# Optimization experiments

Measured on AMD Instinct MI355X. Metric: run time of the kernel, lower is better.

Reference implementation:

```python
import jax, jax.numpy as jnp
import numpy as np

N = 100000   # nodes
E = 1600000  # edges (avg degree 16)
Q = 64       # mesoscale velocity bins
H = 64       # collision MLP hidden dim
DT = 0.1
REG = 1e-6


def setup_inputs() -> dict:
    key = jax.random.key(0)
    ks = jax.random.split(key, 10)
    return {
        "f": jax.random.uniform(ks[0], (N, Q), jnp.float32),
        "macro_u": jax.random.normal(ks[1], (N, 1), jnp.float32),
        "source": 0.01 * jax.random.normal(ks[2], (N, Q), jnp.float32),
        "edge_src": jax.random.randint(ks[3], (E,), 0, N, jnp.int32),
        "edge_dst": jax.random.randint(ks[4], (E,), 0, N, jnp.int32),
        "edge_w": jax.random.uniform(ks[5], (E,), jnp.float32),
        "xi": jnp.linspace(-1.0, 1.0, Q).astype(jnp.float32),
        "w_in": jax.random.normal(ks[6], (Q, H), jnp.float32) / np.float32(np.sqrt(Q)),
        "b_in": jnp.zeros((H,), jnp.float32),
        "w_hid": jax.random.normal(ks[7], (3, H, H), jnp.float32) / np.float32(np.sqrt(H)),
        "b_hid": jnp.zeros((3, H), jnp.float32),
        "w_out": jax.random.normal(ks[8], (H, Q), jnp.float32) / np.float32(np.sqrt(H)),
        "b_out": jnp.zeros((Q,), jnp.float32),
    }


def _collision(f, macro_u, xi, w_in, b_in, w_hid, b_hid, w_out, b_out):
    # 5-layer MLP: relu hidden, tanh output (CollisionOperator.forward)
    x = jax.nn.relu(f @ w_in + b_in)
    for i in range(3):  # fixed small layer count, not a data-dim loop
        x = jax.nn.relu(x @ w_hid[i] + b_hid[i])
    omega = jnp.tanh(x @ w_out + b_out)                     # [N, Q]
    # Hard collision-invariance constraint: Omega* = (I - C^T (C C^T)^-1 C) Omega
    q = f.shape[1]
    w = jnp.full((q,), 1.0 / q, f.dtype)                    # quadrature weights
    xi_shifted = xi[None, :] + macro_u                      # [N, Q]
    C = jnp.stack([jnp.broadcast_to(w, xi_shifted.shape), w * xi_shifted], axis=1)  # [N,2,Q]
    CCT = jnp.einsum('naq,nbq->nab', C, C) + REG * jnp.eye(2, dtype=f.dtype)        # [N,2,2]
    v = jnp.einsum('naq,nq->na', C, omega)                  # [N,2]
    s = jnp.linalg.solve(CCT, v[..., None])[..., 0]         # [N,2]  (== CCT^-1 v)
    return omega - jnp.einsum('naq,na->nq', C, s)           # avoid dense [N,Q,Q] projection


def _transport(f, xi, edge_src, edge_dst, edge_w, n):
    # BoltzmannUpdater.compute_transport_term: both inflow (on graph) and
    # outflow (on reverse graph) reduce to the same per-edge message
    #   m_e = (w_e / out_deg[src_e]) * xi * (f[dst_e] - f[src_e])
    # aggregated at dst (inflow) and at src (outflow); transport = outflow - inflow.
    out_deg = jax.ops.segment_sum(jnp.ones_like(edge_w), edge_src, num_segments=n)
    q_e = edge_w / out_deg[edge_src]                         # [E]
    msg = q_e[:, None] * xi[None, :] * (f[edge_dst] - f[edge_src])  # [E, Q]
    inflow = jax.ops.segment_sum(msg, edge_dst, num_segments=n)
    outflow = jax.ops.segment_sum(msg, edge_src, num_segments=n)
    return outflow - inflow


def reference(f, macro_u, source, edge_src, edge_dst, edge_w, xi,
              w_in, b_in, w_hid, b_hid, w_out, b_out):
    f = jnp.maximum(f, 0.0)  # clamp(min=0)
    omega = _collision(f, macro_u, xi, w_in, b_in, w_hid, b_hid, w_out, b_out)
    trans = _transport(f, xi, edge_src, edge_dst, edge_w, f.shape[0])
    f_new = f - DT * (trans - omega - source)
    return jnp.maximum(f_new, 0.0)
```

## Files before the change

kernel.cpp:

```cpp
#include <hip/hip_runtime.h>

#define NN 100000
#define EE 1600000
#define DTc 0.1f
#define REGc 1e-6f
#define WQc (1.0f / 64.0f)

#define NB 782
#define CAP 4736
#define BCHUNK 16384
#define BS_NB 98
#define ACT_S 72
#define PRE_NB 3125
#define WP_NB 80
#define SIDE_BIT (1u << 24)

typedef unsigned long long u64;
typedef __attribute__((ext_vector_type(8))) short short8;
typedef __attribute__((ext_vector_type(4))) float f32x4;

__device__ __forceinline__ unsigned short f2bf(float x) {
    unsigned u = __float_as_uint(x);
    unsigned r = (u + 0x7fffu + ((u >> 16) & 1u)) >> 16;
    return (unsigned short)r;
}
__device__ __forceinline__ float bf2f(unsigned short s) {
    return __uint_as_float(((unsigned)s) << 16);
}
__device__ __forceinline__ unsigned pack2(float a, float b) {
    return (unsigned)f2bf(fmaxf(a, 0.f)) | ((unsigned)f2bf(fmaxf(b, 0.f)) << 16);
}

__global__ __launch_bounds__(256) void prep_kernel(
    const float* __restrict__ f, unsigned int* __restrict__ fb16u,
    const float* __restrict__ w_in, const float* __restrict__ w_hid,
    const float* __restrict__ w_out, unsigned short* __restrict__ wp,
    const int* __restrict__ esrc, const int* __restrict__ edst,
    const float* __restrict__ ew, int* __restrict__ bcur,
    u64* __restrict__ adj64) {
    int b = blockIdx.x;
    if (b < BS_NB) {
        __shared__ int cnt[NB];
        __shared__ int bas[NB];
        int t = threadIdx.x;
        for (int j = t; j < NB; j += 256) cnt[j] = 0;
        __syncthreads();
        int base = b * BCHUNK;
        int nE = min(BCHUNK, EE - base);
#pragma unroll
        for (int k = 0; k < 8; k++) {
            int i = k * 2048 + t * 8;
            if (i < nE) {
                int4 sa = *(const int4*)&esrc[base + i];
                int4 sb = *(const int4*)&esrc[base + i + 4];
                int4 da = *(const int4*)&edst[base + i];
                int4 db = *(const int4*)&edst[base + i + 4];
                atomicAdd(&cnt[sa.x >> 7], 1); atomicAdd(&cnt[da.x >> 7], 1);
                atomicAdd(&cnt[sa.y >> 7], 1); atomicAdd(&cnt[da.y >> 7], 1);
                atomicAdd(&cnt[sa.z >> 7], 1); atomicAdd(&cnt[da.z >> 7], 1);
                atomicAdd(&cnt[sa.w >> 7], 1); atomicAdd(&cnt[da.w >> 7], 1);
                atomicAdd(&cnt[sb.x >> 7], 1); atomicAdd(&cnt[db.x >> 7], 1);
                atomicAdd(&cnt[sb.y >> 7], 1); atomicAdd(&cnt[db.y >> 7], 1);
                atomicAdd(&cnt[sb.z >> 7], 1); atomicAdd(&cnt[db.z >> 7], 1);
                atomicAdd(&cnt[sb.w >> 7], 1); atomicAdd(&cnt[db.w >> 7], 1);
            }
        }
        __syncthreads();
        for (int j = t; j < NB; j += 256) {
            int c = cnt[j];
            bas[j] = (c ? atomicAdd(&bcur[j], c) : 0) + j * CAP;
            cnt[j] = 0;
        }
        __syncthreads();
#pragma unroll
        for (int k = 0; k < 8; k++) {
            int i = k * 2048 + t * 8;
            if (i < nE) {
                int4 sa = *(const int4*)&esrc[base + i];
                int4 sb = *(const int4*)&esrc[base + i + 4];
                int4 da = *(const int4*)&edst[base + i];
                int4 db = *(const int4*)&edst[base + i + 4];
                float4 wa = *(const float4*)&ew[base + i];
                float4 wb = *(const float4*)&ew[base + i + 4];
#define EMIT(s, d, w)                                                         \
                {                                                             \
                    u64 wb64 = ((u64)__float_as_uint(w)) << 32;               \
                    int p1 = bas[(s) >> 7] + atomicAdd(&cnt[(s) >> 7], 1);    \
                    adj64[p1] = wb64 | SIDE_BIT | (unsigned)((d) | (((s) & 127) << 17)); \
                    int p2 = bas[(d) >> 7] + atomicAdd(&cnt[(d) >> 7], 1);    \
                    adj64[p2] = wb64 | (unsigned)((s) | (((d) & 127) << 17)); \
                }
                EMIT(sa.x, da.x, wa.x) EMIT(sa.y, da.y, wa.y)
                EMIT(sa.z, da.z, wa.z) EMIT(sa.w, da.w, wa.w)
                EMIT(sb.x, db.x, wb.x) EMIT(sb.y, db.y, wb.y)
                EMIT(sb.z, db.z, wb.z) EMIT(sb.w, db.w, wb.w)
#undef EMIT
            }
        }
    } else if (b < BS_NB + PRE_NB) {
        int i = (b - BS_NB) * 256 + threadIdx.x;
        float4 v0 = *(const float4*)&f[i * 8];
        float4 v1 = *(const float4*)&f[i * 8 + 4];
        uint4 w;
        w.x = pack2(v0.x, v0.y);
        w.y = pack2(v0.z, v0.w);
        w.z = pack2(v1.x, v1.y);
        w.w = pack2(v1.z, v1.w);
        *(uint4*)&fb16u[i * 4] = w;
    } else {
        int i = (b - BS_NB - PRE_NB) * 256 + threadIdx.x;
        int l = i >> 12, idx = i & 4095;
        int n = idx >> 6, k = idx & 63;
        const float* W = (l == 0) ? w_in : (l < 4 ? w_hid + (l - 1) * 4096 : w_out);
        wp[i] = f2bf(W[k * 64 + n]);
    }
}

__global__ __launch_bounds__(256) void bucket_histo(
    const int* __restrict__ bcur, const u64* __restrict__ adj64,
    int* __restrict__ node_offs, int* __restrict__ node_end,
    int* __restrict__ deg) {
    __shared__ int cnt_tot[128], cnt_src[128], sc[128];
    int t = threadIdx.x, b = blockIdx.x;
    if (t < 128) { cnt_tot[t] = 0; cnt_src[t] = 0; }
    __syncthreads();
    int used = bcur[b];
    int gstart = b * CAP;
    for (int i = t; i < used; i += 256) {
        unsigned lo = (unsigned)adj64[gstart + i];
        int local = (lo >> 17) & 127;
        atomicAdd(&cnt_tot[local], 1);
        if (lo & SIDE_BIT) atomicAdd(&cnt_src[local], 1);
    }
    __syncthreads();
    if (t < 128) sc[t] = cnt_tot[t];
    __syncthreads();
    for (int o = 1; o < 128; o <<= 1) {
        int x = 0;
        if (t < 128 && t >= o) x = sc[t - o];
        __syncthreads();
        if (t < 128) sc[t] += x;
        __syncthreads();
    }
    if (t < 128) {
        int n = b * 128 + t;
        if (n < NN) {
            node_offs[n] = gstart + sc[t] - cnt_tot[t];
            node_end[n]  = gstart + sc[t];
            deg[n] = cnt_src[t];
        }
    }
}

__global__ __launch_bounds__(256) void bucket_scatter(
    const int* __restrict__ bcur, const u64* __restrict__ adj64,
    const int* __restrict__ node_offs, const int* __restrict__ deg,
    unsigned int* __restrict__ adj4) {
    __shared__ int cur[128];
    __shared__ float ldeg[128];
    int t = threadIdx.x, b = blockIdx.x;
    if (t < 128) {
        int n = b * 128 + t;
        cur[t] = (n < NN) ? node_offs[n] : 0;
        ldeg[t] = (n < NN) ? (float)deg[n] : 1.f;
    }
    __syncthreads();
    int used = bcur[b];
    int gstart = b * CAP;
    for (int i = t; i < used; i += 256) {
        u64 e = adj64[gstart + i];
        unsigned lo = (unsigned)e;
        int local = (lo >> 17) & 127;
        unsigned other = lo & 0x1FFFFu;
        float w = __uint_as_float((unsigned)(e >> 32));
        float dv = (lo & SIDE_BIT) ? ldeg[local] : (float)deg[other];
        float q = w / dv;
        unsigned q15 = (unsigned)(q * 32768.f + 0.5f);
        if (q15 > 32767u) q15 = 32767u;
        int p = atomicAdd(&cur[local], 1);
        adj4[p] = (q15 << 17) | other;
    }
}

#define ACC8(q, r)                                          \
    a0 = fmaf(q, __uint_as_float(r.x << 16), a0);           \
    a1 = fmaf(q, __uint_as_float(r.x & 0xFFFF0000u), a1);   \
    a2 = fmaf(q, __uint_as_float(r.y << 16), a2);           \
    a3 = fmaf(q, __uint_as_float(r.y & 0xFFFF0000u), a3);   \
    a4 = fmaf(q, __uint_as_float(r.z << 16), a4);           \
    a5 = fmaf(q, __uint_as_float(r.z & 0xFFFF0000u), a5);   \
    a6 = fmaf(q, __uint_as_float(r.w << 16), a6);           \
    a7 = fmaf(q, __uint_as_float(r.w & 0xFFFF0000u), a7);   \
    qs += q;

__global__ __launch_bounds__(256) void gather_kernel(
    const unsigned int* __restrict__ fb16u, const int* __restrict__ node_offs,
    const int* __restrict__ node_end,
    const unsigned int* __restrict__ adj, const float* __restrict__ xi,
    float* __restrict__ trans) {
    const float QS = 1.f / 32768.f;
    int lane = threadIdx.x & 63;
    int n = blockIdx.x * 4 + (threadIdx.x >> 6);
    if (n >= NN) return;
    int c = lane & 7;
    int qt = lane >> 3;
    int j = node_offs[n];
    int end = node_end[n];
    float a0 = 0.f, a1 = 0.f, a2 = 0.f, a3 = 0.f;
    float a4 = 0.f, a5 = 0.f, a6 = 0.f, a7 = 0.f, qs = 0.f;
    for (; j + 32 <= end; j += 32) {
        unsigned e0 = __builtin_nontemporal_load(&adj[j + qt]);
        unsigned e1 = __builtin_nontemporal_load(&adj[j + 8 + qt]);
        unsigned e2 = __builtin_nontemporal_load(&adj[j + 16 + qt]);
        unsigned e3 = __builtin_nontemporal_load(&adj[j + 24 + qt]);
        uint4 r0 = *(const uint4*)&fb16u[(e0 & 0x1FFFFu) * 32 + c * 4];
        uint4 r1 = *(const uint4*)&fb16u[(e1 & 0x1FFFFu) * 32 + c * 4];
        uint4 r2 = *(const uint4*)&fb16u[(e2 & 0x1FFFFu) * 32 + c * 4];
        uint4 r3 = *(const uint4*)&fb16u[(e3 & 0x1FFFFu) * 32 + c * 4];
        float q0 = (float)(e0 >> 17) * QS;
        float q1 = (float)(e1 >> 17) * QS;
        float q2 = (float)(e2 >> 17) * QS;
        float q3 = (float)(e3 >> 17) * QS;
        ACC8(q0, r0)
        ACC8(q1, r1)
        ACC8(q2, r2)
        ACC8(q3, r3)
    }
    for (; j + 8 <= end; j += 8) {
        unsigned e = __builtin_nontemporal_load(&adj[j + qt]);
        uint4 r = *(const uint4*)&fb16u[(e & 0x1FFFFu) * 32 + c * 4];
        float q = (float)(e >> 17) * QS;
        ACC8(q, r)
    }
    if (j < end) {
        int idx = j + qt;
        bool ok = idx < end;
        unsigned e = ok ? adj[idx] : 0u;
        uint4 r = *(const uint4*)&fb16u[(e & 0x1FFFFu) * 32 + c * 4];
        float q = ok ? (float)(e >> 17) * QS : 0.f;
        ACC8(q, r)
    }
#define RED3(x) x += __shfl_xor(x, 8); x += __shfl_xor(x, 16); x += __shfl_xor(x, 32)
    RED3(a0); RED3(a1); RED3(a2); RED3(a3);
    RED3(a4); RED3(a5); RED3(a6); RED3(a7); RED3(qs);
    if (qt == 0) {
        uint4 rn = *(const uint4*)&fb16u[n * 32 + c * 4];
        float4 x0 = *(const float4*)&xi[c * 8];
        float4 x1 = *(const float4*)&xi[c * 8 + 4];
        f32x4 o0, o1;
        o0.x = x0.x * (a0 - qs * __uint_as_float(rn.x << 16));
        o0.y = x0.y * (a1 - qs * __uint_as_float(rn.x & 0xFFFF0000u));
        o0.z = x0.z * (a2 - qs * __uint_as_float(rn.y << 16));
        o0.w = x0.w * (a3 - qs * __uint_as_float(rn.y & 0xFFFF0000u));
        o1.x = x1.x * (a4 - qs * __uint_as_float(rn.z << 16));
        o1.y = x1.y * (a5 - qs * __uint_as_float(rn.z & 0xFFFF0000u));
        o1.z = x1.z * (a6 - qs * __uint_as_float(rn.w << 16));
        o1.w = x1.w * (a7 - qs * __uint_as_float(rn.w & 0xFFFF0000u));
        __builtin_nontemporal_store(o0, (f32x4*)&trans[n * 64 + c * 8]);
        __builtin_nontemporal_store(o1, (f32x4*)&trans[n * 64 + c * 8 + 4]);
    }
}

__global__ __launch_bounds__(256) void node_kernel(
    const unsigned short* __restrict__ fb16, const float* __restrict__ f,
    const float* __restrict__ macro_u, const float* __restrict__ source,
    const float* __restrict__ xi, const unsigned short* __restrict__ wp,
    const float* __restrict__ b_in, const float* __restrict__ b_hid,
    const float* __restrict__ b_out,
    const float* __restrict__ trans, float* __restrict__ out) {
    __shared__ __attribute__((aligned(16))) unsigned short act[128 * ACT_S];
    __shared__ float s0s[128], s1s[128], us[128], xif[64];

    const int t = threadIdx.x;
    const int wid = t >> 6;
    const int lane = t & 63;
    const int m = lane & 15;
    const int quad = lane >> 4;
    const int nodeBase = blockIdx.x * 128;
    const int gbase = nodeBase * 64;

    if (t < 128) {
        int n = nodeBase + t;
        us[t] = (n < NN) ? macro_u[n] : 0.f;
    }
    if (t < 64) xif[t] = xi[t];

#pragma unroll
    for (int i = 0; i < 8; i++) {
        int r = wid * 32 + i * 4 + (lane >> 4);
        int c = (lane & 15) * 4;
        uint2 v = {0u, 0u};
        if (nodeBase + r < NN) v = *(const uint2*)&fb16[gbase + r * 64 + c];
        *(uint2*)&act[r * ACT_S + c] = v;
    }

    const int rowbase = wid * 32;

    for (int l = 0; l < 5; l++) {
        const unsigned short* W = wp + l * 4096;
        const float* B = (l == 0) ? b_in : (l < 4 ? b_hid + (l - 1) * 64 : b_out);

        short8 Af[2][2], Bf[4][2];
#pragma unroll
        for (int rt = 0; rt < 2; rt++)
#pragma unroll
            for (int kk = 0; kk < 2; kk++)
                Af[rt][kk] = *(const short8*)&act[(rowbase + rt * 16 + m) * ACT_S + kk * 32 + quad * 8];
#pragma unroll
        for (int ct = 0; ct < 4; ct++)
#pragma unroll
            for (int kk = 0; kk < 2; kk++)
                Bf[ct][kk] = *(const short8*)&W[(ct * 16 + m) * 64 + kk * 32 + quad * 8];

        f32x4 acc[2][4];
#pragma unroll
        for (int rt = 0; rt < 2; rt++)
#pragma unroll
            for (int ct = 0; ct < 4; ct++) {
                acc[rt][ct] = (f32x4){0.f, 0.f, 0.f, 0.f};
                acc[rt][ct] = __builtin_amdgcn_mfma_f32_16x16x32_bf16(Af[rt][0], Bf[ct][0], acc[rt][ct], 0, 0, 0);
                acc[rt][ct] = __builtin_amdgcn_mfma_f32_16x16x32_bf16(Af[rt][1], Bf[ct][1], acc[rt][ct], 0, 0, 0);
            }

#pragma unroll
        for (int rt = 0; rt < 2; rt++)
#pragma unroll
            for (int ct = 0; ct < 4; ct++) {
                float bv = B[ct * 16 + m];
#pragma unroll
                for (int r = 0; r < 4; r++) {
                    int row = rowbase + rt * 16 + quad * 4 + r;
                    float val = acc[rt][ct][r] + bv;
                    val = (l < 4) ? fmaxf(val, 0.f) : tanhf(val);
                    act[row * ACT_S + ct * 16 + m] = f2bf(val);
                }
            }
    }
    __syncthreads();

    if (t < 128) {
        float u = us[t];
        float v0 = 0.f, v1 = 0.f, sxs2 = 0.f, sxi = 0.f;
        const short8* rp = (const short8*)&act[t * ACT_S];
#pragma unroll
        for (int c = 0; c < 8; c++) {
            short8 v = rp[c];
#pragma unroll
            for (int jj = 0; jj < 8; jj++) {
                float om = bf2f((unsigned short)v[jj]);
                float xv = xif[c * 8 + jj];
                float xs = xv + u;
                v0 += om;
                v1 += xs * om;
                sxs2 += xs * xs;
                sxi += xv;
            }
        }
        v0 *= WQc;
        v1 *= WQc;
        float c00 = WQc + REGc;
        float c01 = WQc * WQc * (sxi + 64.f * u);
        float c11 = WQc * WQc * sxs2 + REGc;
        float det = c00 * c11 - c01 * c01;
        float inv = 1.0f / det;
        s0s[t] = (c11 * v0 - c01 * v1) * inv;
        s1s[t] = (c00 * v1 - c01 * v0) * inv;
    }
    __syncthreads();

#pragma unroll
    for (int i = 0; i < 8; i++) {
        int e = (i * 256 + t) * 4;
        int nl = e >> 6;
        if (nodeBase + nl < NN) {
            int g = gbase + e;
            int c0 = e & 63;
            float4 fv = *(const float4*)&f[g];
            float4 sv = *(const float4*)&source[g];
            float4 tv = *(const float4*)&trans[g];
            float uu = us[nl];
            float sv0 = s0s[nl], sv1 = s1s[nl];
            float4 ov;
            float* ovp = (float*)&ov;
            const float* fp = (const float*)&fv;
            const float* sp = (const float*)&sv;
            const float* tp = (const float*)&tv;
#pragma unroll
            for (int jj = 0; jj < 4; jj++) {
                float om = bf2f(act[nl * ACT_S + c0 + jj]);
                float xs = xif[c0 + jj] + uu;
                float omst = om - WQc * (sv0 + xs * sv1);
                float val = fmaxf(fp[jj], 0.f) + DTc * (sp[jj] + omst - tp[jj]);
                ovp[jj] = fmaxf(val, 0.f);
            }
            *(float4*)&out[g] = ov;
        }
    }
}

extern "C" void kernel_launch(void* const* d_in, const int* in_sizes, int n_in,
                              void* d_out, int out_size, void* d_ws, size_t ws_size,
                              hipStream_t stream) {
    const float* f       = (const float*)d_in[0];
    const float* macro_u = (const float*)d_in[1];
    const float* source  = (const float*)d_in[2];
    const int*   esrc    = (const int*)d_in[3];
    const int*   edst    = (const int*)d_in[4];
    const float* ew      = (const float*)d_in[5];
    const float* xi      = (const float*)d_in[6];
    const float* w_in    = (const float*)d_in[7];
    const float* b_in    = (const float*)d_in[8];
    const float* w_hid   = (const float*)d_in[9];
    const float* b_hid   = (const float*)d_in[10];
    const float* w_out   = (const float*)d_in[11];
    const float* b_out   = (const float*)d_in[12];
    float* out = (float*)d_out;

    u64* adj64 = (u64*)d_ws;
    unsigned int* adj4 = (unsigned int*)(adj64 + (size_t)NB * CAP);
    int* deg   = (int*)(adj4 + (size_t)NB * CAP);
    int* node_offs = deg + NN;
    int* node_end  = node_offs + NN;
    int* bcur  = node_end + NN;
    float* trans = (float*)(bcur + 784);
    unsigned short* fb16 = (unsigned short*)(trans + (size_t)NN * 64);
    unsigned short* wp = fb16 + (size_t)NN * 64;

    hipMemsetAsync(bcur, 0, 784 * sizeof(int), stream);

    prep_kernel<<<BS_NB + PRE_NB + WP_NB, 256, 0, stream>>>(
        f, (unsigned int*)fb16, w_in, w_hid, w_out, wp, esrc, edst, ew, bcur, adj64);
    bucket_histo<<<NB, 256, 0, stream>>>(bcur, adj64, node_offs, node_end, deg);
    bucket_scatter<<<NB, 256, 0, stream>>>(bcur, adj64, node_offs, deg, adj4);
    gather_kernel<<<(NN + 3) / 4, 256, 0, stream>>>((const unsigned int*)fb16,
                                                    node_offs, node_end, adj4, xi, trans);
    node_kernel<<<(NN + 127) / 128, 256, 0, stream>>>(
        fb16, f, macro_u, source, xi, wp, b_in, b_hid, b_out, trans, out);
}
```

Measured before the change: 320.1 us.

## Store transport term in bf16 and split edge records into SoA arrays

```diff
diff --git a/kernel.cpp b/kernel.cpp
--- a/kernel.cpp
+++ b/kernel.cpp
@@ -18,6 +18,7 @@
 typedef unsigned long long u64;
 typedef __attribute__((ext_vector_type(8))) short short8;
 typedef __attribute__((ext_vector_type(4))) float f32x4;
+typedef __attribute__((ext_vector_type(4))) unsigned int u32x4;
 
 __device__ __forceinline__ unsigned short f2bf(float x) {
     unsigned u = __float_as_uint(x);
@@ -29,6 +30,9 @@
 }
 __device__ __forceinline__ unsigned pack2(float a, float b) {
     return (unsigned)f2bf(fmaxf(a, 0.f)) | ((unsigned)f2bf(fmaxf(b, 0.f)) << 16);
+}
+__device__ __forceinline__ unsigned pack2raw(float a, float b) {
+    return (unsigned)f2bf(a) | ((unsigned)f2bf(b) << 16);
 }
 
 __global__ __launch_bounds__(256) void prep_kernel(
@@ -37,7 +41,7 @@
     const float* __restrict__ w_out, unsigned short* __restrict__ wp,
     const int* __restrict__ esrc, const int* __restrict__ edst,
     const float* __restrict__ ew, int* __restrict__ bcur,
-    u64* __restrict__ adj64) {
+    unsigned int* __restrict__ lo4, float* __restrict__ w4) {
     int b = blockIdx.x;
     if (b < BS_NB) {
         __shared__ int cnt[NB];
@@ -84,11 +88,12 @@
                 float4 wb = *(const float4*)&ew[base + i + 4];
 #define EMIT(s, d, w)                                                         \
                 {                                                             \
-                    u64 wb64 = ((u64)__float_as_uint(w)) << 32;               \
                     int p1 = bas[(s) >> 7] + atomicAdd(&cnt[(s) >> 7], 1);    \
-                    adj64[p1] = wb64 | SIDE_BIT | (unsigned)((d) | (((s) & 127) << 17)); \
+                    lo4[p1] = SIDE_BIT | (unsigned)((d) | (((s) & 127) << 17)); \
+                    w4[p1] = (w);                                             \
                     int p2 = bas[(d) >> 7] + atomicAdd(&cnt[(d) >> 7], 1);    \
-                    adj64[p2] = wb64 | (unsigned)((s) | (((d) & 127) << 17)); \
+                    lo4[p2] = (unsigned)((s) | (((d) & 127) << 17));          \
+                    w4[p2] = (w);                                             \
                 }
                 EMIT(sa.x, da.x, wa.x) EMIT(sa.y, da.y, wa.y)
                 EMIT(sa.z, da.z, wa.z) EMIT(sa.w, da.w, wa.w)
@@ -117,7 +122,7 @@
 }
 
 __global__ __launch_bounds__(256) void bucket_histo(
-    const int* __restrict__ bcur, const u64* __restrict__ adj64,
+    const int* __restrict__ bcur, const unsigned int* __restrict__ lo4,
     int* __restrict__ node_offs, int* __restrict__ node_end,
     int* __restrict__ deg) {
     __shared__ int cnt_tot[128], cnt_src[128], sc[128];
@@ -127,7 +132,7 @@
     int used = bcur[b];
     int gstart = b * CAP;
     for (int i = t; i < used; i += 256) {
-        unsigned lo = (unsigned)adj64[gstart + i];
+        unsigned lo = lo4[gstart + i];
         int local = (lo >> 17) & 127;
         atomicAdd(&cnt_tot[local], 1);
         if (lo & SIDE_BIT) atomicAdd(&cnt_src[local], 1);
@@ -153,7 +158,8 @@
 }
 
 __global__ __launch_bounds__(256) void bucket_scatter(
-    const int* __restrict__ bcur, const u64* __restrict__ adj64,
+    const int* __restrict__ bcur, const unsigned int* __restrict__ lo4,
+    const float* __restrict__ w4,
     const int* __restrict__ node_offs, const int* __restrict__ deg,
     unsigned int* __restrict__ adj4) {
     __shared__ int cur[128];
@@ -168,11 +174,10 @@
     int used = bcur[b];
     int gstart = b * CAP;
     for (int i = t; i < used; i += 256) {
-        u64 e = adj64[gstart + i];
-        unsigned lo = (unsigned)e;
+        unsigned lo = lo4[gstart + i];
+        float w = w4[gstart + i];
         int local = (lo >> 17) & 127;
         unsigned other = lo & 0x1FFFFu;
-        float w = __uint_as_float((unsigned)(e >> 32));
         float dv = (lo & SIDE_BIT) ? ldeg[local] : (float)deg[other];
         float q = w / dv;
         unsigned q15 = (unsigned)(q * 32768.f + 0.5f);
@@ -197,7 +202,7 @@
     const unsigned int* __restrict__ fb16u, const int* __restrict__ node_offs,
     const int* __restrict__ node_end,
     const unsigned int* __restrict__ adj, const float* __restrict__ xi,
-    float* __restrict__ trans) {
+    unsigned int* __restrict__ transb) {
     const float QS = 1.f / 32768.f;
     int lane = threadIdx.x & 63;
     int n = blockIdx.x * 4 + (threadIdx.x >> 6);
@@ -247,17 +252,20 @@
         uint4 rn = *(const uint4*)&fb16u[n * 32 + c * 4];
         float4 x0 = *(const float4*)&xi[c * 8];
         float4 x1 = *(const float4*)&xi[c * 8 + 4];
-        f32x4 o0, o1;
-        o0.x = x0.x * (a0 - qs * __uint_as_float(rn.x << 16));
-        o0.y = x0.y * (a1 - qs * __uint_as_float(rn.x & 0xFFFF0000u));
-        o0.z = x0.z * (a2 - qs * __uint_as_float(rn.y << 16));
-        o0.w = x0.w * (a3 - qs * __uint_as_float(rn.y & 0xFFFF0000u));
-        o1.x = x1.x * (a4 - qs * __uint_as_float(rn.z << 16));
-        o1.y = x1.y * (a5 - qs * __uint_as_float(rn.z & 0xFFFF0000u));
-        o1.z = x1.z * (a6 - qs * __uint_as_float(rn.w << 16));
-        o1.w = x1.w * (a7 - qs * __uint_as_float(rn.w & 0xFFFF0000u));
-        __builtin_nontemporal_store(o0, (f32x4*)&trans[n * 64 + c * 8]);
-        __builtin_nontemporal_store(o1, (f32x4*)&trans[n * 64 + c * 8 + 4]);
+        float t0 = x0.x * (a0 - qs * __uint_as_float(rn.x << 16));
+        float t1 = x0.y * (a1 - qs * __uint_as_float(rn.x & 0xFFFF0000u));
+        float t2 = x0.z * (a2 - qs * __uint_as_float(rn.y << 16));
+        float t3 = x0.w * (a3 - qs * __uint_as_float(rn.y & 0xFFFF0000u));
+        float t4 = x1.x * (a4 - qs * __uint_as_float(rn.z << 16));
+        float t5 = x1.y * (a5 - qs * __uint_as_float(rn.z & 0xFFFF0000u));
+        float t6 = x1.z * (a6 - qs * __uint_as_float(rn.w << 16));
+        float t7 = x1.w * (a7 - qs * __uint_as_float(rn.w & 0xFFFF0000u));
+        u32x4 ov;
+        ov.x = pack2raw(t0, t1);
+        ov.y = pack2raw(t2, t3);
+        ov.z = pack2raw(t4, t5);
+        ov.w = pack2raw(t6, t7);
+        __builtin_nontemporal_store(ov, (u32x4*)&transb[n * 32 + c * 4]);
     }
 }
 
@@ -267,7 +275,7 @@
     const float* __restrict__ xi, const unsigned short* __restrict__ wp,
     const float* __restrict__ b_in, const float* __restrict__ b_hid,
     const float* __restrict__ b_out,
-    const float* __restrict__ trans, float* __restrict__ out) {
+    const unsigned int* __restrict__ transb, float* __restrict__ out) {
     __shared__ __attribute__((aligned(16))) unsigned short act[128 * ACT_S];
     __shared__ float s0s[128], s1s[128], us[128], xif[64];
 
@@ -377,20 +385,24 @@
             int c0 = e & 63;
             float4 fv = *(const float4*)&f[g];
             float4 sv = *(const float4*)&source[g];
-            float4 tv = *(const float4*)&trans[g];
+            uint2 tvb = *(const uint2*)&transb[g >> 1];
             float uu = us[nl];
             float sv0 = s0s[nl], sv1 = s1s[nl];
+            float tpv[4];
+            tpv[0] = bf2f((unsigned short)(tvb.x & 0xFFFFu));
+            tpv[1] = bf2f((unsigned short)(tvb.x >> 16));
+            tpv[2] = bf2f((unsigned short)(tvb.y & 0xFFFFu));
+            tpv[3] = bf2f((unsigned short)(tvb.y >> 16));
             float4 ov;
             float* ovp = (float*)&ov;
             const float* fp = (const float*)&fv;
             const float* sp = (const float*)&sv;
-            const float* tp = (const float*)&tv;
 #pragma unroll
             for (int jj = 0; jj < 4; jj++) {
                 float om = bf2f(act[nl * ACT_S + c0 + jj]);
                 float xs = xif[c0 + jj] + uu;
                 float omst = om - WQc * (sv0 + xs * sv1);
-                float val = fmaxf(fp[jj], 0.f) + DTc * (sp[jj] + omst - tp[jj]);
+                float val = fmaxf(fp[jj], 0.f) + DTc * (sp[jj] + omst - tpv[jj]);
                 ovp[jj] = fmaxf(val, 0.f);
             }
             *(float4*)&out[g] = ov;
@@ -416,24 +428,26 @@
     const float* b_out   = (const float*)d_in[12];
     float* out = (float*)d_out;
 
-    u64* adj64 = (u64*)d_ws;
-    unsigned int* adj4 = (unsigned int*)(adj64 + (size_t)NB * CAP);
+    unsigned int* lo4 = (unsigned int*)d_ws;
+    float* w4 = (float*)(lo4 + (size_t)NB * CAP);
+    unsigned int* adj4 = (unsigned int*)(w4 + (size_t)NB * CAP);
     int* deg   = (int*)(adj4 + (size_t)NB * CAP);
     int* node_offs = deg + NN;
     int* node_end  = node_offs + NN;
     int* bcur  = node_end + NN;
-    float* trans = (float*)(bcur + 784);
-    unsigned short* fb16 = (unsigned short*)(trans + (size_t)NN * 64);
+    unsigned int* transb = (unsigned int*)(bcur + 784);
+    unsigned short* fb16 = (unsigned short*)(transb + (size_t)NN * 32);
     unsigned short* wp = fb16 + (size_t)NN * 64;
 
-    hipMemsetAsync(bcur, 0, 784 * sizeof(int), stream);
+    (void)hipMemsetAsync(bcur, 0, 784 * sizeof(int), stream);
 
     prep_kernel<<<BS_NB + PRE_NB + WP_NB, 256, 0, stream>>>(
-        f, (unsigned int*)fb16, w_in, w_hid, w_out, wp, esrc, edst, ew, bcur, adj64);
-    bucket_histo<<<NB, 256, 0, stream>>>(bcur, adj64, node_offs, node_end, deg);
-    bucket_scatter<<<NB, 256, 0, stream>>>(bcur, adj64, node_offs, deg, adj4);
+        f, (unsigned int*)fb16, w_in, w_hid, w_out, wp, esrc, edst, ew, bcur,
+        lo4, w4);
+    bucket_histo<<<NB, 256, 0, stream>>>(bcur, lo4, node_offs, node_end, deg);
+    bucket_scatter<<<NB, 256, 0, stream>>>(bcur, lo4, w4, node_offs, deg, adj4);
     gather_kernel<<<(NN + 3) / 4, 256, 0, stream>>>((const unsigned int*)fb16,
-                                                    node_offs, node_end, adj4, xi, trans);
+                                                    node_offs, node_end, adj4, xi, transb);
     node_kernel<<<(NN + 127) / 128, 256, 0, stream>>>(
-        fb16, f, macro_u, source, xi, wp, b_in, b_hid, b_out, trans, out);
-}
+        fb16, f, macro_u, source, xi, wp, b_in, b_hid, b_out, transb, out);
+}
```

Result: slower. 361.3 us (+12.9%).
